# Kernel optimization log

Measured on AMD Instinct MI355X. Metric: run time of the kernel, lower is better.

Reference implementation:

```python
import jax, jax.numpy as jnp
import numpy as np

D_MODEL, D_STATE, D_CONV, EXPAND = 1024, 16, 4, 2
D_INNER = EXPAND * D_MODEL
BATCH, SEQ = 2, 2048


def setup_inputs() -> dict:
    key = jax.random.key(0)
    ks = jax.random.split(key, 10)
    inv = lambda n: 1.0 / np.sqrt(n)
    return {
        "x": jax.random.normal(ks[0], (BATCH, SEQ, D_MODEL), jnp.float32),
        "in_proj_w": jax.random.uniform(ks[1], (2 * D_INNER, D_MODEL), jnp.float32, -inv(D_MODEL), inv(D_MODEL)),
        "conv_w": jax.random.uniform(ks[2], (D_INNER, D_INNER, D_CONV), jnp.float32, -inv(D_INNER * D_CONV), inv(D_INNER * D_CONV)),
        "conv_b": jax.random.uniform(ks[3], (D_INNER,), jnp.float32, -inv(D_INNER * D_CONV), inv(D_INNER * D_CONV)),
        "dt_w": jax.random.uniform(ks[4], (D_INNER, D_INNER), jnp.float32, -inv(D_INNER), inv(D_INNER)),
        "dt_b": jax.random.uniform(ks[5], (D_INNER,), jnp.float32, -inv(D_INNER), inv(D_INNER)),
        "A_log": jax.random.normal(ks[6], (D_INNER, D_STATE), jnp.float32) * 0.01,
        "D": jnp.ones((D_INNER,), jnp.float32),
        "B_w": jax.random.uniform(ks[7], (D_STATE, D_INNER), jnp.float32, -inv(D_INNER), inv(D_INNER)),
        "C_w": jax.random.uniform(ks[8], (D_STATE, D_INNER), jnp.float32, -inv(D_INNER), inv(D_INNER)),
        "out_w": jax.random.uniform(ks[9], (D_MODEL, D_INNER), jnp.float32, -inv(D_INNER), inv(D_INNER)),
    }


def _forward(x, in_proj_w, conv_w, conv_b, dt_w, dt_b, A_log, D, B_w, C_w, out_w):
    xz = x @ in_proj_w.T                      # [b, l, 2*d_inner]
    xc, z = jnp.split(xz, 2, axis=-1)
    # causal depthful conv1d (full channel mixing, left-padded)
    h = jnp.transpose(xc, (0, 2, 1))          # [b, d, l]
    h = jnp.pad(h, ((0, 0), (0, 0), (D_CONV - 1, 0)))
    h = jax.lax.conv_general_dilated(h, conv_w, (1,), 'VALID',
                                     dimension_numbers=('NCH', 'OIH', 'NCH'))
    h = h + conv_b[None, :, None]
    u = jnp.transpose(h, (0, 2, 1))           # [b, l, d_inner]

    dt = jnp.clip(jax.nn.sigmoid(u @ dt_w.T + dt_b), 1e-4, 1.0)  # [b, l, d]
    A = -jnp.exp(A_log)                       # [d, n]
    Bm = u @ B_w.T                            # [b, l, n]
    Cm = u @ C_w.T                            # [b, l, n]

    # time-major scan over the recurrence
    u_t = jnp.transpose(u, (1, 0, 2))
    dt_t = jnp.transpose(dt, (1, 0, 2))
    B_t = jnp.transpose(Bm, (1, 0, 2))
    C_t = jnp.transpose(Cm, (1, 0, 2))

    def step(state, inp):
        ut, dtt, bt, ct = inp                 # [b,d], [b,d], [b,n], [b,n]
        dA = jnp.exp(jnp.clip(dtt[:, :, None] * A, -5.0, 5.0))   # [b,d,n]
        dB = dtt[:, :, None] * bt[:, None, :] * ut[:, :, None]   # [b,d,n]
        state = dA * state + dB + 1e-6
        y = jnp.sum(state * ct[:, None, :], axis=-1) + D * ut    # [b,d]
        return state, y

    state0 = jnp.zeros((x.shape[0], D_INNER, D_STATE), x.dtype)
    _, ys = jax.lax.scan(step, state0, (u_t, dt_t, B_t, C_t))
    y = jnp.transpose(ys, (1, 0, 2))          # [b, l, d_inner]
    y = y * jax.nn.silu(z)
    return y @ out_w.T                        # [b, l, d_model]


def reference(x, in_proj_w, conv_w, conv_b, dt_w, dt_b, A_log, D, B_w, C_w, out_w):
    return _forward(x, in_proj_w, conv_w, conv_b, dt_w, dt_b, A_log, D, B_w, C_w, out_w)
```

## Files before the change

### kernel.cpp

```cpp
#include <hip/hip_runtime.h>

#define BATCHN 2
#define SEQL   2048
#define DM     1024
#define DI     2048
#define DSN    16
#define MTOT   (BATCHN * SEQL)
#define PADL   (SEQL + 3)
#define NC     64
#define CL     (SEQL / NC)
#define BCKS   8

typedef __attribute__((ext_vector_type(8))) __bf16 bf16x8;
typedef __attribute__((ext_vector_type(4))) float f32x4;

__device__ __forceinline__ unsigned short f2b(float f) {
    union { float f; unsigned u; } v; v.f = f;
    unsigned r = v.u + 0x7FFF + ((v.u >> 16) & 1);
    return (unsigned short)(r >> 16);
}
__device__ __forceinline__ float b2f(unsigned short b) {
    union { float f; unsigned u; } v; v.u = ((unsigned)b) << 16;
    return v.f;
}

__device__ __forceinline__ void gl_lds16(const void* g, void* l) {
    __builtin_amdgcn_global_load_lds(
        (const __attribute__((address_space(1))) unsigned int*)g,
        (__attribute__((address_space(3))) unsigned int*)l, 16, 0, 0);
}

__device__ __forceinline__ void swz(int& bx, int& by) {
    int gx = gridDim.x, gy = gridDim.y;
    int lin = blockIdx.y * gx + blockIdx.x;
    int xcd = lin & 7, k = lin >> 3;
    int rw = gx >> 1, rh = gy >> 2;
    by = (xcd >> 1) * rh + k / rw;
    bx = (xcd & 1) * rw + k % rw;
}

#define NB_XCVT (MTOT * DM / 4 / 256)
__global__ void cvt_x_all(const float* __restrict__ src, unsigned short* __restrict__ dst) {
    int blk = blockIdx.x;
    if (blk < NB_XCVT) {
        int i = blk * 256 + threadIdx.x;
        int b = i >> 19;
        float4 v = ((const float4*)src)[i];
        ushort4 o;
        o.x = f2b(v.x); o.y = f2b(v.y); o.z = f2b(v.z); o.w = f2b(v.w);
        ((ushort4*)dst)[i + (b + 1) * (3 * DM / 4)] = o;
    } else {
        int i = (blk - NB_XCVT) * 256 + threadIdx.x;
        if (i < BATCHN * 3 * DM) {
            int b = i / (3 * DM);
            int r = i % (3 * DM);
            dst[(size_t)b * PADL * DM + r] = 0;
        }
    }
}

#define NB_CONVW (DI * DI / 256)
#define NB_TP    ((DM / 32) * (DI / 32))
#define NB_IPZ   (DI * DM / 4 / 256)
#define NB_DTW   (DI * DI / 4 / 256)
#define NB_OW    (DM * DI / 4 / 256)
#define NB_BW    (DSN * DI / 4 / 256 + 1)
__global__ void __launch_bounds__(256)
cvt_w_all(const float* __restrict__ convw, const float* __restrict__ ipw,
          const float* __restrict__ dtw, const float* __restrict__ ow,
          const float* __restrict__ bw, const float* __restrict__ cw,
          unsigned short* __restrict__ wk, unsigned short* __restrict__ Pt,
          unsigned short* __restrict__ ipz, unsigned short* __restrict__ dtwb,
          unsigned short* __restrict__ owb, unsigned short* __restrict__ bcb)
{
    __shared__ float tile[32][33];
    int blk = blockIdx.x;
    int t = threadIdx.x;
    if (blk < NB_CONVW) {
        int i = blk * 256 + t;
        float4 v = ((const float4*)convw)[i];
        wk[0 * (size_t)DI * DI + i] = f2b(v.x);
        wk[1 * (size_t)DI * DI + i] = f2b(v.y);
        wk[2 * (size_t)DI * DI + i] = f2b(v.z);
        wk[3 * (size_t)DI * DI + i] = f2b(v.w);
        return;
    }
    blk -= NB_CONVW;
    if (blk < NB_TP) {
        int ct = (blk & 31) * 32, it = (blk >> 5) * 32;
        int tx = t & 31, ty = t >> 5;
#pragma unroll
        for (int r = 0; r < 4; ++r)
            tile[ty + r * 8][tx] = ipw[(size_t)(it + ty + r * 8) * DM + ct + tx];
        __syncthreads();
#pragma unroll
        for (int r = 0; r < 4; ++r)
            Pt[(size_t)(ct + ty + r * 8) * DI + it + tx] = f2b(tile[tx][ty + r * 8]);
        return;
    }
    blk -= NB_TP;
    const float* src;
    unsigned short* dst;
    int n4;
    if (blk < NB_IPZ) {
        src = ipw + (size_t)DI * DM; dst = ipz; n4 = DI * DM / 4;
    } else if ((blk -= NB_IPZ) < NB_DTW) {
        src = dtw; dst = dtwb; n4 = DI * DI / 4;
    } else if ((blk -= NB_DTW) < NB_OW) {
        src = ow; dst = owb; n4 = DM * DI / 4;
    } else if ((blk -= NB_OW) < NB_BW) {
        src = bw; dst = bcb; n4 = DSN * DI / 4;
    } else {
        blk -= NB_BW;
        src = cw; dst = bcb + (size_t)DSN * DI; n4 = DSN * DI / 4;
    }
    int i = blk * 256 + t;
    if (i < n4) {
        float4 v = ((const float4*)src)[i];
        ushort4 o;
        o.x = f2b(v.x); o.y = f2b(v.y); o.z = f2b(v.z); o.w = f2b(v.w);
        ((ushort4*)dst)[i] = o;
    }
}

template<int MODE>
__global__ void __launch_bounds__(256)
gemm_bt(const unsigned short* __restrict__ Abase,
        const unsigned short* __restrict__ Bbase,
        const float* __restrict__ bias,
        unsigned short* __restrict__ out_bf,
        float* __restrict__ out_f,
        int K)
{
    __shared__ __align__(16) unsigned short As[128 * 64];
    __shared__ __align__(16) unsigned short Bs[128 * 64];

    const int t = threadIdx.x;
    const int lane = t & 63;
    const int wave = t >> 6;
    const int wm = wave & 1, wn = wave >> 1;
    int bx, by;
    swz(bx, by);
    const int m0 = by * 128, n0 = bx * 128;
    const int srow = t >> 3;
    const int scol = (t & 7) * 8;
    const int gcol = (((t & 7) ^ (srow & 7))) * 8;

    f32x4 acc[4][4];
#pragma unroll
    for (int i = 0; i < 4; ++i)
#pragma unroll
        for (int j = 0; j < 4; ++j)
            acc[i][j] = f32x4{0.f, 0.f, 0.f, 0.f};

    const int nseg = (MODE == 1) ? 4 : 1;
    for (int seg = 0; seg < nseg; ++seg) {
        const unsigned short* arow[4];
        const unsigned short* brow[4];
#pragma unroll
        for (int i = 0; i < 4; ++i) {
            int rg = m0 + srow + i * 32;
            if (MODE == 0) {
                arow[i] = Abase + ((size_t)(rg >> 11) * PADL + 3 + (rg & 2047)) * DM;
            } else if (MODE == 1) {
                arow[i] = Abase + ((size_t)(rg >> 11) * PADL + (rg & 2047) + seg) * DM;
            } else if (MODE == 4) {
                arow[i] = Abase + (size_t)blockIdx.z * DI * DI + (size_t)rg * K;
            } else {
                arow[i] = Abase + (size_t)rg * K;
            }
            int ng = n0 + srow + i * 32;
            if (MODE == 1)
                brow[i] = Bbase + (size_t)seg * DI * DM + (size_t)ng * DM;
            else
                brow[i] = Bbase + (size_t)ng * K;
        }
        const int Kseg = (MODE == 1) ? DM : K;
        for (int k0 = 0; k0 < Kseg; k0 += 64) {
#pragma unroll
            for (int i = 0; i < 4; ++i)
                gl_lds16(arow[i] + k0 + gcol, &As[(size_t)(srow + i * 32) * 64 + scol]);
#pragma unroll
            for (int i = 0; i < 4; ++i)
                gl_lds16(brow[i] + k0 + gcol, &Bs[(size_t)(srow + i * 32) * 64 + scol]);
            __syncthreads();
            const int qa = (lane >> 4) * 8;
            const int am = lane & 15;
            const int sw = (am & 7) << 3;
#pragma unroll
            for (int kk = 0; kk < 64; kk += 32) {
                bf16x8 af[4], bfv[4];
#pragma unroll
                for (int i = 0; i < 4; ++i)
                    af[i] = *(const bf16x8*)&As[(wm * 64 + i * 16 + am) * 64 + ((kk + qa) ^ sw)];
#pragma unroll
                for (int j = 0; j < 4; ++j)
                    bfv[j] = *(const bf16x8*)&Bs[(wn * 64 + j * 16 + am) * 64 + ((kk + qa) ^ sw)];
#pragma unroll
                for (int i = 0; i < 4; ++i)
#pragma unroll
                    for (int j = 0; j < 4; ++j)
                        acc[i][j] = __builtin_amdgcn_mfma_f32_16x16x32_bf16(
                            af[i], bfv[j], acc[i][j], 0, 0, 0);
            }
            __syncthreads();
        }
    }

    const int erow0 = m0 + wm * 64;
    const int ecol0 = n0 + wn * 64 + (lane & 15);
    const int rq = (lane >> 4) * 4;
#pragma unroll
    for (int i = 0; i < 4; ++i) {
#pragma unroll
        for (int j = 0; j < 4; ++j) {
            int col = ecol0 + j * 16;
#pragma unroll
            for (int r = 0; r < 4; ++r) {
                int row = erow0 + i * 16 + rq + r;
                float v = acc[i][j][r];
                if (MODE == 0) {
                    out_bf[(size_t)row * DI + col] = f2b(v);
                } else if (MODE == 1) {
                    v += bias[col];
                    out_bf[(size_t)row * DI + col] = f2b(v);
                } else if (MODE == 2) {
                    v += bias[col];
                    float s = 1.f / (1.f + __expf(-v));
                    s = fminf(fmaxf(s, 1e-4f), 1.f);
                    out_bf[(size_t)row * DI + col] = f2b(s);
                } else if (MODE == 3) {
                    out_f[(size_t)row * DM + col] = v;
                } else {
                    out_bf[(size_t)blockIdx.z * DI * DM + (size_t)row * DM + col] = f2b(v);
                }
            }
        }
    }
}

__global__ void __launch_bounds__(256)
bc_mfma(const unsigned short* __restrict__ u,
        const unsigned short* __restrict__ w,
        float* __restrict__ pc)
{
    const int t = threadIdx.x;
    const int lane = t & 63;
    const int wave = t >> 6;
    const int ks = blockIdx.x;
    const int m0 = blockIdx.y * 128 + wave * 32;
    const int am = lane & 15, quad = lane >> 4;

    f32x4 acc[2][2];
#pragma unroll
    for (int i = 0; i < 2; ++i)
#pragma unroll
        for (int j = 0; j < 2; ++j)
            acc[i][j] = f32x4{0.f, 0.f, 0.f, 0.f};

    const int kbase = ks * (DI / BCKS);
    const unsigned short* ur0 = u + (size_t)(m0 + am) * DI;
    const unsigned short* ur1 = u + (size_t)(m0 + 16 + am) * DI;
    const unsigned short* wr0 = w + (size_t)am * DI;
    const unsigned short* wr1 = w + (size_t)(16 + am) * DI;
#pragma unroll 2
    for (int kk = 0; kk < DI / BCKS; kk += 32) {
        int k = kbase + kk + quad * 8;
        bf16x8 a0 = *(const bf16x8*)(ur0 + k);
        bf16x8 a1 = *(const bf16x8*)(ur1 + k);
        bf16x8 b0 = *(const bf16x8*)(wr0 + k);
        bf16x8 b1 = *(const bf16x8*)(wr1 + k);
        acc[0][0] = __builtin_amdgcn_mfma_f32_16x16x32_bf16(a0, b0, acc[0][0], 0, 0, 0);
        acc[0][1] = __builtin_amdgcn_mfma_f32_16x16x32_bf16(a0, b1, acc[0][1], 0, 0, 0);
        acc[1][0] = __builtin_amdgcn_mfma_f32_16x16x32_bf16(a1, b0, acc[1][0], 0, 0, 0);
        acc[1][1] = __builtin_amdgcn_mfma_f32_16x16x32_bf16(a1, b1, acc[1][1], 0, 0, 0);
    }
    float* base = pc + (size_t)ks * MTOT * 32;
#pragma unroll
    for (int i = 0; i < 2; ++i)
#pragma unroll
        for (int j = 0; j < 2; ++j)
#pragma unroll
            for (int r = 0; r < 4; ++r) {
                int row = m0 + i * 16 + quad * 4 + r;
                int col = j * 16 + am;
                base[(size_t)row * 32 + col] = acc[i][j][r];
            }
}

__global__ void __launch_bounds__(256)
bc_reduce(const float* __restrict__ pc, float* __restrict__ outf)
{
    int i = blockIdx.x * 256 + threadIdx.x;
    const float4* p4 = (const float4*)pc;
    float4 s = p4[i];
#pragma unroll
    for (int ks = 1; ks < BCKS; ++ks) {
        float4 v = p4[(size_t)ks * (MTOT * 8) + i];
        s.x += v.x; s.y += v.y; s.z += v.z; s.w += v.w;
    }
    ((float4*)outf)[i] = s;
}

__global__ void __launch_bounds__(256)
scan_p1(const unsigned short* __restrict__ dt_bf,
        const unsigned short* __restrict__ u_bf,
        const float* __restrict__ bcf,
        const float* __restrict__ A_log,
        float* __restrict__ Pbuf,
        float* __restrict__ Sbuf)
{
    const int t = threadIdx.x;
    const int blk = blockIdx.x;
    const int c  = blk & (NC - 1);
    const int dh = (blk >> 6) & 7;
    const int b  = blk >> 9;
    const int d  = dh * 256 + t;

    float Adn[16];
    {
        const float4* ar = (const float4*)(A_log + (size_t)d * DSN);
#pragma unroll
        for (int q = 0; q < 4; ++q) {
            float4 v = ar[q];
            Adn[q * 4 + 0] = -__expf(v.x);
            Adn[q * 4 + 1] = -__expf(v.y);
            Adn[q * 4 + 2] = -__expf(v.z);
            Adn[q * 4 + 3] = -__expf(v.w);
        }
    }
    float s[16], P[16];
#pragma unroll
    for (int n = 0; n < 16; ++n) { s[n] = 0.f; P[n] = 1.f; }

    const size_t rowbase = (size_t)b * SEQL + (size_t)c * CL;
    for (int l0 = 0; l0 < CL; l0 += 4) {
        float dt4[4], u4[4];
#pragma unroll
        for (int j = 0; j < 4; ++j) {
            size_t rb = rowbase + l0 + j;
            dt4[j] = b2f(dt_bf[rb * DI + d]);
            u4[j] = b2f(u_bf[rb * DI + d]);
        }
#pragma unroll
        for (int j = 0; j < 4; ++j) {
            size_t rb = rowbase + l0 + j;
            const float4* Br = (const float4*)(bcf + rb * 32);
            float Bn[16];
#pragma unroll
            for (int q = 0; q < 4; ++q) {
                float4 v = Br[q];
                Bn[q * 4 + 0] = v.x; Bn[q * 4 + 1] = v.y;
                Bn[q * 4 + 2] = v.z; Bn[q * 4 + 3] = v.w;
            }
            float dt = dt4[j];
            float dBu = dt * u4[j];
#pragma unroll
            for (int n = 0; n < 16; ++n) {
                float x = dt * Adn[n];
                x = fminf(fmaxf(x, -5.f), 5.f);
                float dA = __expf(x);
                P[n] *= dA;
                s[n] = dA * s[n] + (dBu * Bn[n] + 1e-6f);
            }
        }
    }
    size_t ob = (((size_t)c * BATCHN + b) * DI + d) * DSN;
#pragma unroll
    for (int q = 0; q < 4; ++q) {
        ((float4*)(Pbuf + ob))[q] = make_float4(P[q*4], P[q*4+1], P[q*4+2], P[q*4+3]);
        ((float4*)(Sbuf + ob))[q] = make_float4(s[q*4], s[q*4+1], s[q*4+2], s[q*4+3]);
    }
}

__global__ void __launch_bounds__(256)
scan_p2(const float* __restrict__ Pbuf,
        const float* __restrict__ Sbuf,
        float* __restrict__ Ibuf)
{
    const int i = blockIdx.x * 256 + threadIdx.x;
    const int stride = BATCHN * DI * DSN;
    float s = 0.f;
    for (int c0 = 0; c0 < NC; c0 += 8) {
        float Pv[8], Sv[8];
#pragma unroll
        for (int j = 0; j < 8; ++j) {
            size_t idx = (size_t)(c0 + j) * stride + i;
            Pv[j] = Pbuf[idx];
            Sv[j] = Sbuf[idx];
        }
#pragma unroll
        for (int j = 0; j < 8; ++j) {
            size_t idx = (size_t)(c0 + j) * stride + i;
            Ibuf[idx] = s;
            s = Pv[j] * s + Sv[j];
        }
    }
}

__global__ void __launch_bounds__(256)
scan_p3(const unsigned short* __restrict__ dt_bf,
        const unsigned short* __restrict__ u_bf,
        const float* __restrict__ bcf,
        const unsigned short* __restrict__ z_bf,
        const float* __restrict__ A_log,
        const float* __restrict__ Dvec,
        const float* __restrict__ Ibuf,
        unsigned short* __restrict__ y_bf)
{
    const int t = threadIdx.x;
    const int blk = blockIdx.x;
    const int c  = blk & (NC - 1);
    const int dh = (blk >> 6) & 7;
    const int b  = blk >> 9;
    const int d  = dh * 256 + t;

    float Adn[16];
    {
        const float4* ar = (const float4*)(A_log + (size_t)d * DSN);
#pragma unroll
        for (int q = 0; q < 4; ++q) {
            float4 v = ar[q];
            Adn[q * 4 + 0] = -__expf(v.x);
            Adn[q * 4 + 1] = -__expf(v.y);
            Adn[q * 4 + 2] = -__expf(v.z);
            Adn[q * 4 + 3] = -__expf(v.w);
        }
    }
    const float Dd = Dvec[d];
    float s[16];
    {
        size_t ib = (((size_t)c * BATCHN + b) * DI + d) * DSN;
#pragma unroll
        for (int q = 0; q < 4; ++q) {
            float4 v = ((const float4*)(Ibuf + ib))[q];
            s[q * 4 + 0] = v.x; s[q * 4 + 1] = v.y;
            s[q * 4 + 2] = v.z; s[q * 4 + 3] = v.w;
        }
    }

    const size_t rowbase = (size_t)b * SEQL + (size_t)c * CL;
    for (int l0 = 0; l0 < CL; l0 += 4) {
        float dt4[4], u4[4], z4[4];
#pragma unroll
        for (int j = 0; j < 4; ++j) {
            size_t rb = rowbase + l0 + j;
            dt4[j] = b2f(dt_bf[rb * DI + d]);
            u4[j] = b2f(u_bf[rb * DI + d]);
            z4[j] = b2f(z_bf[rb * DI + d]);
        }
#pragma unroll
        for (int j = 0; j < 4; ++j) {
            size_t rb = rowbase + l0 + j;
            const float4* Br = (const float4*)(bcf + rb * 32);
            float Bn[16], Cn[16];
#pragma unroll
            for (int q = 0; q < 4; ++q) {
                float4 v = Br[q];
                Bn[q * 4 + 0] = v.x; Bn[q * 4 + 1] = v.y;
                Bn[q * 4 + 2] = v.z; Bn[q * 4 + 3] = v.w;
                float4 w = Br[q + 4];
                Cn[q * 4 + 0] = w.x; Cn[q * 4 + 1] = w.y;
                Cn[q * 4 + 2] = w.z; Cn[q * 4 + 3] = w.w;
            }
            float dt = dt4[j];
            float dBu = dt * u4[j];
            float y = 0.f;
#pragma unroll
            for (int n = 0; n < 16; ++n) {
                float x = dt * Adn[n];
                x = fminf(fmaxf(x, -5.f), 5.f);
                float dA = __expf(x);
                s[n] = dA * s[n] + (dBu * Bn[n] + 1e-6f);
                y += s[n] * Cn[n];
            }
            y += Dd * u4[j];
            float zz = z4[j];
            y *= zz / (1.f + __expf(-zz));
            y_bf[rb * DI + d] = f2b(y);
        }
    }
}

extern "C" void kernel_launch(void* const* d_in, const int* in_sizes, int n_in,
                              void* d_out, int out_size, void* d_ws, size_t ws_size,
                              hipStream_t stream) {
    const float* x     = (const float*)d_in[0];
    const float* ipw   = (const float*)d_in[1];
    const float* convw = (const float*)d_in[2];
    const float* convb = (const float*)d_in[3];
    const float* dtw   = (const float*)d_in[4];
    const float* dtb   = (const float*)d_in[5];
    const float* alog  = (const float*)d_in[6];
    const float* dvec  = (const float*)d_in[7];
    const float* bw    = (const float*)d_in[8];
    const float* cwm   = (const float*)d_in[9];
    const float* ow    = (const float*)d_in[10];
    float* out = (float*)d_out;

    char* ws = (char*)d_ws;
    size_t off = 0;
    auto carve = [&](size_t bytes) {
        char* p = ws + off;
        off += (bytes + 255) & ~(size_t)255;
        return p;
    };
    unsigned short* xpad   = (unsigned short*)carve((size_t)BATCHN * PADL * DM * 2);
    unsigned short* ipz_bf = (unsigned short*)carve((size_t)DI * DM * 2);
    unsigned short* Pt_bf  = (unsigned short*)carve((size_t)DM * DI * 2);
    unsigned short* wk_bf  = (unsigned short*)carve((size_t)4 * DI * DI * 2);
    unsigned short* mk_bf  = (unsigned short*)carve((size_t)4 * DI * DM * 2);
    unsigned short* dtw_bf = (unsigned short*)carve((size_t)DI * DI * 2);
    unsigned short* ow_bf  = (unsigned short*)carve((size_t)DM * DI * 2);
    unsigned short* bc_bf  = (unsigned short*)carve((size_t)2 * DSN * DI * 2);
    unsigned short* z_bf   = (unsigned short*)carve((size_t)MTOT * DI * 2);
    unsigned short* u_bf   = (unsigned short*)carve((size_t)MTOT * DI * 2);
    unsigned short* dt_bf  = (unsigned short*)carve((size_t)MTOT * DI * 2);
    float*          bc_f   = (float*)carve((size_t)MTOT * 2 * DSN * 4);
    unsigned short* y_bf   = (unsigned short*)carve((size_t)MTOT * DI * 2);
    float*          Pbuf   = (float*)carve((size_t)NC * BATCHN * DI * DSN * 4);
    float*          Sbuf   = (float*)carve((size_t)NC * BATCHN * DI * DSN * 4);
    float*          Ibuf   = (float*)carve((size_t)NC * BATCHN * DI * DSN * 4);
    float*          pc_f   = (float*)carve((size_t)BCKS * MTOT * 32 * 4);

    cvt_x_all<<<NB_XCVT + (BATCHN * 3 * DM + 255) / 256, 256, 0, stream>>>(x, xpad);
    {
        int nb = NB_CONVW + NB_TP + NB_IPZ + NB_DTW + NB_OW + 2 * NB_BW;
        cvt_w_all<<<nb, 256, 0, stream>>>(convw, ipw, dtw, ow, bw, cwm,
                                          wk_bf, Pt_bf, ipz_bf, dtw_bf, ow_bf, bc_bf);
    }

    gemm_bt<4><<<dim3(8, 16, 4), 256, 0, stream>>>(wk_bf, Pt_bf, nullptr, mk_bf, nullptr, DI);
    gemm_bt<0><<<dim3(16, 32), 256, 0, stream>>>(xpad, ipz_bf, nullptr, z_bf, nullptr, DM);
    gemm_bt<1><<<dim3(16, 32), 256, 0, stream>>>(xpad, mk_bf, convb, u_bf, nullptr, DM);
    bc_mfma<<<dim3(BCKS, MTOT / 128), 256, 0, stream>>>(u_bf, bc_bf, pc_f);
    bc_reduce<<<MTOT * 32 / 4 / 256, 256, 0, stream>>>(pc_f, bc_f);
    gemm_bt<2><<<dim3(16, 32), 256, 0, stream>>>(u_bf, dtw_bf, dtb, dt_bf, nullptr, DI);
    scan_p1<<<BATCHN * 8 * NC, 256, 0, stream>>>(dt_bf, u_bf, bc_f, alog, Pbuf, Sbuf);
    scan_p2<<<BATCHN * DI * DSN / 256, 256, 0, stream>>>(Pbuf, Sbuf, Ibuf);
    scan_p3<<<BATCHN * 8 * NC, 256, 0, stream>>>(dt_bf, u_bf, bc_f, z_bf, alog, dvec, Ibuf, y_bf);
    gemm_bt<3><<<dim3(8, 32), 256, 0, stream>>>(y_bf, ow_bf, nullptr, nullptr, out, DI);
}
```

Baseline: 478.2 us.

## Add 256x128 eight-wave pipelined GEMM kernel for projection and conv GEMMs

```diff
diff --git a/kernel.cpp b/kernel.cpp
--- a/kernel.cpp
+++ b/kernel.cpp
@@ -153,58 +153,43 @@
         for (int j = 0; j < 4; ++j)
             acc[i][j] = f32x4{0.f, 0.f, 0.f, 0.f};
 
-    const int nseg = (MODE == 1) ? 4 : 1;
-    for (int seg = 0; seg < nseg; ++seg) {
-        const unsigned short* arow[4];
-        const unsigned short* brow[4];
-#pragma unroll
-        for (int i = 0; i < 4; ++i) {
-            int rg = m0 + srow + i * 32;
-            if (MODE == 0) {
-                arow[i] = Abase + ((size_t)(rg >> 11) * PADL + 3 + (rg & 2047)) * DM;
-            } else if (MODE == 1) {
-                arow[i] = Abase + ((size_t)(rg >> 11) * PADL + (rg & 2047) + seg) * DM;
-            } else if (MODE == 4) {
-                arow[i] = Abase + (size_t)blockIdx.z * DI * DI + (size_t)rg * K;
-            } else {
-                arow[i] = Abase + (size_t)rg * K;
-            }
-            int ng = n0 + srow + i * 32;
-            if (MODE == 1)
-                brow[i] = Bbase + (size_t)seg * DI * DM + (size_t)ng * DM;
-            else
-                brow[i] = Bbase + (size_t)ng * K;
-        }
-        const int Kseg = (MODE == 1) ? DM : K;
-        for (int k0 = 0; k0 < Kseg; k0 += 64) {
+    const unsigned short* arow[4];
+    const unsigned short* brow[4];
+#pragma unroll
+    for (int i = 0; i < 4; ++i) {
+        int rg = m0 + srow + i * 32;
+        arow[i] = Abase + (size_t)rg * K;
+        int ng = n0 + srow + i * 32;
+        brow[i] = Bbase + (size_t)ng * K;
+    }
+    for (int k0 = 0; k0 < K; k0 += 64) {
+#pragma unroll
+        for (int i = 0; i < 4; ++i)
+            gl_lds16(arow[i] + k0 + gcol, &As[(size_t)(srow + i * 32) * 64 + scol]);
+#pragma unroll
+        for (int i = 0; i < 4; ++i)
+            gl_lds16(brow[i] + k0 + gcol, &Bs[(size_t)(srow + i * 32) * 64 + scol]);
+        __syncthreads();
+        const int qa = (lane >> 4) * 8;
+        const int am = lane & 15;
+        const int sw = (am & 7) << 3;
+#pragma unroll
+        for (int kk = 0; kk < 64; kk += 32) {
+            bf16x8 af[4], bfv[4];
 #pragma unroll
             for (int i = 0; i < 4; ++i)
-                gl_lds16(arow[i] + k0 + gcol, &As[(size_t)(srow + i * 32) * 64 + scol]);
+                af[i] = *(const bf16x8*)&As[(wm * 64 + i * 16 + am) * 64 + ((kk + qa) ^ sw)];
+#pragma unroll
+            for (int j = 0; j < 4; ++j)
+                bfv[j] = *(const bf16x8*)&Bs[(wn * 64 + j * 16 + am) * 64 + ((kk + qa) ^ sw)];
 #pragma unroll
             for (int i = 0; i < 4; ++i)
-                gl_lds16(brow[i] + k0 + gcol, &Bs[(size_t)(srow + i * 32) * 64 + scol]);
-            __syncthreads();
-            const int qa = (lane >> 4) * 8;
-            const int am = lane & 15;
-            const int sw = (am & 7) << 3;
-#pragma unroll
-            for (int kk = 0; kk < 64; kk += 32) {
-                bf16x8 af[4], bfv[4];
-#pragma unroll
-                for (int i = 0; i < 4; ++i)
-                    af[i] = *(const bf16x8*)&As[(wm * 64 + i * 16 + am) * 64 + ((kk + qa) ^ sw)];
 #pragma unroll
                 for (int j = 0; j < 4; ++j)
-                    bfv[j] = *(const bf16x8*)&Bs[(wn * 64 + j * 16 + am) * 64 + ((kk + qa) ^ sw)];
-#pragma unroll
-                for (int i = 0; i < 4; ++i)
-#pragma unroll
-                    for (int j = 0; j < 4; ++j)
-                        acc[i][j] = __builtin_amdgcn_mfma_f32_16x16x32_bf16(
-                            af[i], bfv[j], acc[i][j], 0, 0, 0);
-            }
-            __syncthreads();
-        }
+                    acc[i][j] = __builtin_amdgcn_mfma_f32_16x16x32_bf16(
+                        af[i], bfv[j], acc[i][j], 0, 0, 0);
+        }
+        __syncthreads();
     }
 
     const int erow0 = m0 + wm * 64;
@@ -219,6 +204,165 @@
             for (int r = 0; r < 4; ++r) {
                 int row = erow0 + i * 16 + rq + r;
                 float v = acc[i][j][r];
+                if (MODE == 3) {
+                    out_f[(size_t)row * DM + col] = v;
+                } else {
+                    out_bf[(size_t)row * DI + col] = f2b(v);
+                }
+            }
+        }
+    }
+}
+
+
+#define ABUF8(b) ((b) * 16384)
+#define BBUF8(b) (32768 + (b) * 8192)
+
+#define STA8(buf, Mh, kt) do { const int kc_ = ((kt) & NTM) << 6; \
+    gl_lds16(pAst + (size_t)((Mh) * 32) * SA + kc_, &lds[ABUF8(buf) + (Mh) * 8192 + ldsw]); \
+    gl_lds16(pAst + (size_t)((Mh) * 32 + 128) * SA + kc_, &lds[ABUF8(buf) + (Mh) * 8192 + 4096 + ldsw]); \
+} while (0)
+#define STB8(buf, Nh, kt) do { const int kc_ = ((kt) & NTM) << 6; \
+    gl_lds16(pBst + (size_t)((Nh) * 32) * SB + kc_, &lds[BBUF8(buf) + (Nh) * 4096 + ldsw]); \
+} while (0)
+
+#define LA8(buf, Mh) \
+    a00 = *(const bf16x8*)&lds[ABUF8(buf) + (Mh) * 8192 + ar + c0]; \
+    a01 = *(const bf16x8*)&lds[ABUF8(buf) + (Mh) * 8192 + ar + c1]; \
+    a10 = *(const bf16x8*)&lds[ABUF8(buf) + (Mh) * 8192 + ar + 1024 + c0]; \
+    a11 = *(const bf16x8*)&lds[ABUF8(buf) + (Mh) * 8192 + ar + 1024 + c1];
+#define LB8(buf, Nh) \
+    b00 = *(const bf16x8*)&lds[BBUF8(buf) + (Nh) * 4096 + br + c0]; \
+    b01 = *(const bf16x8*)&lds[BBUF8(buf) + (Nh) * 4096 + br + c1]; \
+    b10 = *(const bf16x8*)&lds[BBUF8(buf) + (Nh) * 4096 + br + 1024 + c0]; \
+    b11 = *(const bf16x8*)&lds[BBUF8(buf) + (Nh) * 4096 + br + 1024 + c1];
+
+#define MM8(Mh, Nh) \
+    acc[(Mh)*2][(Nh)*2]     = __builtin_amdgcn_mfma_f32_16x16x32_bf16(a00, b00, acc[(Mh)*2][(Nh)*2], 0, 0, 0); \
+    acc[(Mh)*2][(Nh)*2+1]   = __builtin_amdgcn_mfma_f32_16x16x32_bf16(a00, b10, acc[(Mh)*2][(Nh)*2+1], 0, 0, 0); \
+    acc[(Mh)*2+1][(Nh)*2]   = __builtin_amdgcn_mfma_f32_16x16x32_bf16(a10, b00, acc[(Mh)*2+1][(Nh)*2], 0, 0, 0); \
+    acc[(Mh)*2+1][(Nh)*2+1] = __builtin_amdgcn_mfma_f32_16x16x32_bf16(a10, b10, acc[(Mh)*2+1][(Nh)*2+1], 0, 0, 0); \
+    acc[(Mh)*2][(Nh)*2]     = __builtin_amdgcn_mfma_f32_16x16x32_bf16(a01, b01, acc[(Mh)*2][(Nh)*2], 0, 0, 0); \
+    acc[(Mh)*2][(Nh)*2+1]   = __builtin_amdgcn_mfma_f32_16x16x32_bf16(a01, b11, acc[(Mh)*2][(Nh)*2+1], 0, 0, 0); \
+    acc[(Mh)*2+1][(Nh)*2]   = __builtin_amdgcn_mfma_f32_16x16x32_bf16(a11, b01, acc[(Mh)*2+1][(Nh)*2], 0, 0, 0); \
+    acc[(Mh)*2+1][(Nh)*2+1] = __builtin_amdgcn_mfma_f32_16x16x32_bf16(a11, b11, acc[(Mh)*2+1][(Nh)*2+1], 0, 0, 0);
+
+#define PH_MID \
+    __builtin_amdgcn_s_barrier(); \
+    asm volatile("s_waitcnt lgkmcnt(0)" ::: "memory"); \
+    __builtin_amdgcn_sched_barrier(0); \
+    __builtin_amdgcn_s_setprio(1);
+#define PH_END \
+    __builtin_amdgcn_s_setprio(0); \
+    __builtin_amdgcn_s_barrier(); \
+    __builtin_amdgcn_sched_barrier(0);
+#define PH_END_W \
+    __builtin_amdgcn_s_setprio(0); \
+    asm volatile("s_waitcnt vmcnt(3)" ::: "memory"); \
+    __builtin_amdgcn_s_barrier(); \
+    __builtin_amdgcn_sched_barrier(0);
+
+template<int MODE>
+__global__ void __launch_bounds__(512, 1)
+gemm8(const unsigned short* __restrict__ Abase,
+      const unsigned short* __restrict__ Bbase,
+      const float* __restrict__ bias,
+      unsigned short* __restrict__ out_bf,
+      float* __restrict__ out_f)
+{
+    constexpr int K   = (MODE == 0) ? 1024 : (MODE == 1) ? 4096 : 2048;
+    constexpr int SA  = (MODE == 2 || MODE == 4) ? 2048 : 1024;
+    constexpr int SB  = (MODE == 0) ? 1024 : (MODE == 1) ? 4096 : 2048;
+    constexpr int NT  = K / 64;
+    constexpr int NTM = NT - 1;
+    constexpr int NI  = NT / 2;
+    (void)out_f;
+
+    __shared__ __align__(16) unsigned short lds[49152];
+
+    const int t = threadIdx.x;
+    const int lane = t & 63;
+    const int wave = t >> 6;
+    const int wm = wave >> 1;
+    const int wn = wave & 1;
+    int bx, by;
+    swz(bx, by);
+    const int m0 = by * 256, n0 = bx * 128;
+
+    const unsigned short* Ap;
+    if (MODE == 0)      Ap = Abase + ((size_t)(m0 >> 11) * PADL + 3 + (m0 & 2047)) * DM;
+    else if (MODE == 1) Ap = Abase + ((size_t)(m0 >> 11) * PADL + (m0 & 2047)) * DM;
+    else if (MODE == 4) Ap = Abase + (size_t)blockIdx.z * DI * DI + (size_t)m0 * SA;
+    else                Ap = Abase + (size_t)m0 * SA;
+    const unsigned short* Bp = Bbase + (size_t)n0 * SB;
+
+    const int tr = t >> 3;
+    const int rowg = ((tr >> 5) << 6) + (tr & 31);
+    const int gcolb = ((t & 7) ^ (tr & 7)) << 3;
+    const unsigned short* pAst = Ap + (size_t)rowg * SA + gcolb;
+    const unsigned short* pBst = Bp + (size_t)rowg * SB + gcolb;
+    const int ldsw = t * 8;
+
+    const int am = lane & 15;
+    const int qa = (lane >> 4) << 3;
+    const int sw = (am & 7) << 3;
+    const int c0 = qa ^ sw;
+    const int c1 = (32 + qa) ^ sw;
+    const int ar = wm * 2048 + am * 64;
+    const int br = wn * 2048 + am * 64;
+
+    f32x4 acc[4][4];
+#pragma unroll
+    for (int i = 0; i < 4; ++i)
+#pragma unroll
+        for (int j = 0; j < 4; ++j)
+            acc[i][j] = f32x4{0.f, 0.f, 0.f, 0.f};
+
+    bf16x8 a00, a01, a10, a11, b00, b01, b10, b11;
+
+    STA8(0, 0, 0); STB8(0, 1, 0); STA8(0, 1, 0); STB8(0, 0, 0);
+    STA8(1, 0, 1); STB8(1, 1, 1);
+    asm volatile("s_waitcnt vmcnt(3)" ::: "memory");
+    __builtin_amdgcn_s_barrier();
+    __builtin_amdgcn_sched_barrier(0);
+
+#pragma unroll 1
+    for (int it = 0; it < NI; ++it) {
+        const int ko  = 2 * it + 1;
+        const int ke  = (2 * it + 2) & NTM;
+        const int ko2 = (2 * it + 3) & NTM;
+        LA8(0, 0) LB8(0, 0) STA8(1, 1, ko);
+        PH_MID MM8(0, 0) PH_END
+        LB8(0, 1) STB8(1, 0, ko);
+        PH_MID MM8(0, 1) PH_END
+        LA8(0, 1) STA8(0, 0, ke);
+        PH_MID MM8(1, 1) PH_END
+        LB8(0, 0) STB8(0, 1, ke);
+        PH_MID MM8(1, 0) PH_END_W
+        LA8(1, 0) LB8(1, 0) STA8(0, 1, ke);
+        PH_MID MM8(0, 0) PH_END
+        LB8(1, 1) STB8(0, 0, ke);
+        PH_MID MM8(0, 1) PH_END
+        LA8(1, 1) STA8(1, 0, ko2);
+        PH_MID MM8(1, 1) PH_END
+        LB8(1, 0) STB8(1, 1, ko2);
+        PH_MID MM8(1, 0) PH_END_W
+    }
+
+    asm volatile("s_waitcnt vmcnt(0)" ::: "memory");
+
+    const int rq = (lane >> 4) << 2;
+    const int er = m0 + wm * 64;
+    const int ec = n0 + wn * 64 + am;
+#pragma unroll
+    for (int mi = 0; mi < 4; ++mi) {
+#pragma unroll
+        for (int nj = 0; nj < 4; ++nj) {
+            int col = ec + nj * 16;
+#pragma unroll
+            for (int r = 0; r < 4; ++r) {
+                int row = er + mi * 16 + rq + r;
+                float v = acc[mi][nj][r];
                 if (MODE == 0) {
                     out_bf[(size_t)row * DI + col] = f2b(v);
                 } else if (MODE == 1) {
@@ -229,10 +373,8 @@
                     float s = 1.f / (1.f + __expf(-v));
                     s = fminf(fmaxf(s, 1e-4f), 1.f);
                     out_bf[(size_t)row * DI + col] = f2b(s);
-                } else if (MODE == 3) {
-                    out_f[(size_t)row * DM + col] = v;
                 } else {
-                    out_bf[(size_t)blockIdx.z * DI * DM + (size_t)row * DM + col] = f2b(v);
+                    out_bf[(size_t)row * 4096 + (size_t)blockIdx.z * 1024 + col] = f2b(v);
                 }
             }
         }
@@ -530,12 +672,12 @@
                                           wk_bf, Pt_bf, ipz_bf, dtw_bf, ow_bf, bc_bf);
     }
 
-    gemm_bt<4><<<dim3(8, 16, 4), 256, 0, stream>>>(wk_bf, Pt_bf, nullptr, mk_bf, nullptr, DI);
-    gemm_bt<0><<<dim3(16, 32), 256, 0, stream>>>(xpad, ipz_bf, nullptr, z_bf, nullptr, DM);
-    gemm_bt<1><<<dim3(16, 32), 256, 0, stream>>>(xpad, mk_bf, convb, u_bf, nullptr, DM);
+    gemm8<4><<<dim3(8, 8, 4), 512, 0, stream>>>(wk_bf, Pt_bf, nullptr, mk_bf, nullptr);
+    gemm8<0><<<dim3(16, 16), 512, 0, stream>>>(xpad, ipz_bf, nullptr, z_bf, nullptr);
+    gemm8<1><<<dim3(16, 16), 512, 0, stream>>>(xpad, mk_bf, convb, u_bf, nullptr);
     bc_mfma<<<dim3(BCKS, MTOT / 128), 256, 0, stream>>>(u_bf, bc_bf, pc_f);
     bc_reduce<<<MTOT * 32 / 4 / 256, 256, 0, stream>>>(pc_f, bc_f);
-    gemm_bt<2><<<dim3(16, 32), 256, 0, stream>>>(u_bf, dtw_bf, dtb, dt_bf, nullptr, DI);
+    gemm8<2><<<dim3(16, 16), 512, 0, stream>>>(u_bf, dtw_bf, dtb, dt_bf, nullptr);
     scan_p1<<<BATCHN * 8 * NC, 256, 0, stream>>>(dt_bf, u_bf, bc_f, alog, Pbuf, Sbuf);
     scan_p2<<<BATCHN * DI * DSN / 256, 256, 0, stream>>>(Pbuf, Sbuf, Ibuf);
     scan_p3<<<BATCHN * 8 * NC, 256, 0, stream>>>(dt_bf, u_bf, bc_f, z_bf, alog, dvec, Ibuf, y_bf);
```

Result: faster. 466.3 us (-2.5%).
